# Performance work log

Measured on AMD Instinct MI355X. Metric: run time of the kernel, lower is better.

## Reference

```python
import jax, jax.numpy as jnp
import numpy as np

HEADS = 16
DIM_HEAD = 64
BLOCK = 16
SEQ_LEN = 2048
NUM_BLOCKS = SEQ_LEN // BLOCK  # 128
NUM_RANDOM_BLOCKS = 32
LOCAL_WINDOW = 4
GLOBAL_BLOCKS = [0]


def make_layout():
    # Deterministic stand-in for DeepSpeed VariableSparsityConfig.make_layout
    # (local windows of 4 blocks + random blocks + global block columns/rows,
    #  then tril for unidirectional attention).
    rng = np.random.RandomState(0)
    nb = NUM_BLOCKS
    layout = np.zeros((nb, nb), dtype=bool)
    for w in range(0, nb, LOCAL_WINDOW):
        layout[w:w + LOCAL_WINDOW, w:w + LOCAL_WINDOW] = True
    rnd = rng.randint(0, nb, size=(nb, NUM_RANDOM_BLOCKS))
    layout[np.arange(nb)[:, None], rnd] = True
    for g in GLOBAL_BLOCKS:
        layout[:, g] = True
        layout[g, :] = True
    layout = np.tril(layout)  # unidirectional
    return jnp.asarray(layout)


def setup_inputs() -> dict:
    key = jax.random.key(0)
    k1, k2, k3 = jax.random.split(key, 3)
    dim = 1024
    inner = HEADS * DIM_HEAD  # 1024
    x = jax.random.normal(k1, (2, SEQ_LEN, dim), dtype=jnp.float32)
    w_qkv = jax.random.normal(k2, (dim, 3 * inner), dtype=jnp.float32) * 0.02
    w_out = jax.random.normal(k3, (inner, dim), dtype=jnp.float32) * 0.02
    b_out = jnp.zeros((dim,), dtype=jnp.float32)
    layout = make_layout()  # [128, 128] bool
    return {"x": x, "w_qkv": w_qkv, "w_out": w_out, "b_out": b_out, "layout": layout}


def reference(x, w_qkv, w_out, b_out, layout):
    b, n, _ = x.shape
    scale = DIM_HEAD ** -0.5
    qkv = x @ w_qkv  # [b, n, 3*h*d]
    q, k, v = jnp.split(qkv, 3, axis=-1)
    split_heads = lambda t: t.reshape(b, n, HEADS, DIM_HEAD).transpose(0, 2, 1, 3)
    q, k, v = split_heads(q), split_heads(k), split_heads(v)  # [b, h, n, d]

    scores = jnp.einsum('bhid,bhjd->bhij', q, k) * scale  # [b, h, n, n]
    neg = -jnp.finfo(scores.dtype).max
    # additive causal attn_mask (value = -finfo.max / 2, attn_mask_mode='add')
    causal = jnp.triu(jnp.ones((n, n), dtype=bool), 1)
    scores = scores + jnp.where(causal, neg / 2, jnp.zeros((), scores.dtype))
    # block-sparse layout: entries outside allowed blocks are fully masked
    allowed = jnp.repeat(jnp.repeat(layout, BLOCK, axis=0), BLOCK, axis=1)  # [n, n]
    scores = jnp.where(allowed, scores, neg)
    attn = jax.nn.softmax(scores, axis=-1)
    out = jnp.einsum('bhij,bhjd->bhid', attn, v)  # [b, h, n, d]
    out = out.transpose(0, 2, 1, 3).reshape(b, n, HEADS * DIM_HEAD)
    return out @ w_out + b_out
```

## Files before the change

### kernel.cpp

```cpp
#include <hip/hip_runtime.h>
#include <cstdint>
#include <cstddef>


typedef short bf8 __attribute__((ext_vector_type(8)));
typedef float f32x4 __attribute__((ext_vector_type(4)));
typedef unsigned short u16;
typedef unsigned int u32;

#define MFMA_BF16(a, b, c) __builtin_amdgcn_mfma_f32_16x16x32_bf16((a), (b), (c), 0, 0, 0)

constexpr int SEQ = 2048;
constexpr int NH = 16;
constexpr int DHD = 64;
constexpr int NBLK = 128;
constexpr int DIM = 1024;

__device__ __forceinline__ u16 f2bf(float f) {
  unsigned u = __float_as_uint(f);
  return (u16)((u + 0x7fffu + ((u >> 16) & 1u)) >> 16);
}
__device__ __forceinline__ u32 pack2bf(float a, float b) {
  return (u32)f2bf(a) | ((u32)f2bf(b) << 16);
}
__device__ __forceinline__ void gload_lds16(const u16* g, u16* l) {
  auto gp = (const __attribute__((address_space(1))) u16*)(g);
  auto lp = (__attribute__((address_space(3))) u16*)(l);
  __builtin_amdgcn_global_load_lds(gp, lp, 16, 0, 0);
}

__global__ __launch_bounds__(256) void prep(
    const float* __restrict__ x, u16* __restrict__ xbf,
    const float* __restrict__ wqkv, u16* __restrict__ wqkvT,
    const float* __restrict__ wout, u16* __restrict__ woutT,
    const unsigned char* __restrict__ lay,
    int* __restrict__ cnt, int* __restrict__ cols) {
  __shared__ u16 tile[64][72];
  int bid = blockIdx.x;
  int t = threadIdx.x;

  if (bid < 2048) {
    int idx = (bid * 256 + t) * 8;
    float4 a = *(const float4*)(x + idx);
    float4 b = *(const float4*)(x + idx + 4);
    *(ushort4*)(xbf + idx)     = make_ushort4(f2bf(a.x), f2bf(a.y), f2bf(a.z), f2bf(a.w));
    *(ushort4*)(xbf + idx + 4) = make_ushort4(f2bf(b.x), f2bf(b.y), f2bf(b.z), f2bf(b.w));
    return;
  }
  bid -= 2048;
  if (bid < 768 + 256) {
    const float* in; u16* out; int C, bx, by;
    if (bid < 768) { in = wqkv; out = wqkvT; C = 3072; bx = bid % 48; by = bid / 48; }
    else { int r = bid - 768; in = wout; out = woutT; C = 1024; bx = r % 16; by = r / 16; }
    const int R = 1024;
    int c0 = bx * 64, r0 = by * 64;
    int rr = t >> 4, cc = (t & 15) * 4;
    #pragma unroll
    for (int p = 0; p < 64; p += 16) {
      float4 v = *(const float4*)(in + (size_t)(r0 + rr + p) * C + c0 + cc);
      tile[rr + p][cc + 0] = f2bf(v.x);
      tile[rr + p][cc + 1] = f2bf(v.y);
      tile[rr + p][cc + 2] = f2bf(v.z);
      tile[rr + p][cc + 3] = f2bf(v.w);
    }
    __syncthreads();
    int oc = t >> 3, orr = (t & 7) * 8;
    #pragma unroll
    for (int p = 0; p < 64; p += 32) {
      u16 tmp[8];
      #pragma unroll
      for (int qy = 0; qy < 8; qy++) tmp[qy] = tile[orr + qy][oc + p];
      u16* dst = out + (size_t)(c0 + oc + p) * R + r0 + orr;
      *(ushort4*)(dst)     = make_ushort4(tmp[0], tmp[1], tmp[2], tmp[3]);
      *(ushort4*)(dst + 4) = make_ushort4(tmp[4], tmp[5], tmp[6], tmp[7]);
    }
    return;
  }
  bid -= 1024;
  int wave = t >> 6, lane = t & 63;
  int i = bid * 4 + wave;
  const uint4* l4 = (const uint4*)lay;
  u32 acc = 0;
  #pragma unroll
  for (int it = 0; it < 16; it++) {
    uint4 v = l4[it * 64 + lane];
    acc |= ((v.x | v.y | v.z | v.w) & 0xFFFFFF00u);
  }
  bool as_int32 = (__ballot(acc != 0) == 0ULL);
  const int* li = (const int*)lay;
  int j0 = lane, j1 = lane + 64;
  bool p0 = (j0 <= i) && (as_int32 ? (li[i * 128 + j0] != 0) : (lay[i * 128 + j0] != 0));
  bool p1 = (j1 <= i) && (as_int32 ? (li[i * 128 + j1] != 0) : (lay[i * 128 + j1] != 0));
  unsigned long long m0 = __ballot(p0), m1 = __ballot(p1);
  unsigned long long lt = (1ULL << lane) - 1ULL;
  int base0 = __popcll(m0);
  if (p0) cols[i * 128 + __popcll(m0 & lt)] = j0;
  if (p1) cols[i * 128 + base0 + __popcll(m1 & lt)] = j1;
  if (lane == 0) cnt[i] = base0 + __popcll(m1);
}

__global__ __launch_bounds__(256) void gemm_qkv(
    const u16* __restrict__ A, const u16* __restrict__ Bt,
    u16* __restrict__ oq, u16* __restrict__ okk, u16* __restrict__ ov) {
  __shared__ u16 smem[16896];
  u16* sA = smem;
  u16* sB = smem + 8192;
  const int K = 1024;
  int tid = threadIdx.x, lane = tid & 63, wave = tid >> 6;
  int quad = lane >> 4, l16 = lane & 15;
  int wr = wave >> 1, wc = wave & 1;
  int bm0 = blockIdx.y * 128, bn0 = blockIdx.x * 128;

  f32x4 acc[4][4];
  #pragma unroll
  for (int i = 0; i < 4; i++)
    #pragma unroll
    for (int j = 0; j < 4; j++) acc[i][j] = (f32x4){0.f, 0.f, 0.f, 0.f};

  int srow8 = lane >> 3;
  int schunk = ((lane & 7) ^ srow8) * 8;
  for (int k0 = 0; k0 < K; k0 += 64) {
    #pragma unroll
    for (int r = 0; r < 4; r++) {
      int row = wave * 8 + r * 32 + srow8;
      gload_lds16(A + (size_t)(bm0 + row) * K + k0 + schunk,
                  sA + (wave * 8 + r * 32) * 64);
    }
    #pragma unroll
    for (int r = 0; r < 4; r++) {
      int row = wave * 8 + r * 32 + srow8;
      gload_lds16(Bt + (size_t)(bn0 + row) * K + k0 + schunk,
                  sB + (wave * 8 + r * 32) * 64);
    }
    __syncthreads();
    #pragma unroll
    for (int ks = 0; ks < 2; ks++) {
      bf8 af[4], bfr[4];
      #pragma unroll
      for (int i = 0; i < 4; i++) {
        int phys = ((ks * 4 + quad) ^ (l16 & 7)) * 8;
        af[i] = *(const bf8*)(sA + (wr * 64 + i * 16 + l16) * 64 + phys);
      }
      #pragma unroll
      for (int j = 0; j < 4; j++) {
        int phys = ((ks * 4 + quad) ^ (l16 & 7)) * 8;
        bfr[j] = *(const bf8*)(sB + (wc * 64 + j * 16 + l16) * 64 + phys);
      }
      #pragma unroll
      for (int i = 0; i < 4; i++)
        #pragma unroll
        for (int j = 0; j < 4; j++)
          acc[i][j] = MFMA_BF16(af[i], bfr[j], acc[i][j]);
    }
    __syncthreads();
  }

  int which = bn0 >> 10;
  if (which == 2) {
    #pragma unroll
    for (int j = 0; j < 4; j++) {
      int c = bn0 + wc * 64 + j * 16 + l16;
      int h = (c & 1023) >> 6, dd = c & 63;
      #pragma unroll
      for (int i = 0; i < 4; i++) {
        int r0 = bm0 + wr * 64 + i * 16;
        int b = r0 >> 11, nn0 = r0 & 2047, jb = nn0 >> 4;
        u16* dst = ov + ((size_t)((b * NH + h) * NBLK + jb) * DHD + dd) * 16 + quad * 4;
        *(ushort4*)dst = make_ushort4(f2bf(acc[i][j][0]), f2bf(acc[i][j][1]),
                                      f2bf(acc[i][j][2]), f2bf(acc[i][j][3]));
      }
    }
  } else {
    u16* dstbase = (which == 0) ? oq : okk;
    #pragma unroll
    for (int j = 0; j < 4; j++) {
      int col = wc * 64 + j * 16 + l16;
      #pragma unroll
      for (int i = 0; i < 4; i++) {
        int row = wr * 64 + i * 16 + quad * 4;
        *(uint2*)&smem[col * 132 + row] =
            make_uint2(pack2bf(acc[i][j][0], acc[i][j][1]),
                       pack2bf(acc[i][j][2], acc[i][j][3]));
      }
    }
    __syncthreads();
    int r = tid >> 1, half = tid & 1;
    int rglob = bm0 + r;
    int b = rglob >> 11, nn = rglob & 2047;
    int h = ((bn0 & 1023) >> 6) + half;
    #pragma unroll
    for (int j = 0; j < 4; j++) {
      union { u16 t[16]; uint4 q[2]; } tv;
      #pragma unroll
      for (int dd = 0; dd < 16; dd++)
        tv.t[dd] = smem[(half * 64 + j * 16 + dd) * 132 + r];
      u16* dst = dstbase + ((size_t)(b * NH + h) * SEQ + nn) * DHD + j * 16;
      *(uint4*)(dst) = tv.q[0];
      *(uint4*)(dst + 8) = tv.q[1];
    }
  }
}

__global__ __launch_bounds__(256) void gemm_out(
    const u16* __restrict__ A, const u16* __restrict__ Bt,
    float* __restrict__ of, const float* __restrict__ bias) {
  __shared__ u16 smem[12288];
  u16* sA = smem;
  u16* sB = smem + 8192;
  const int K = 1024, N = 1024;
  int tid = threadIdx.x, lane = tid & 63, wave = tid >> 6;
  int quad = lane >> 4, l16 = lane & 15;
  int wr = wave >> 1, wc = wave & 1;
  int bm0 = blockIdx.y * 128, bn0 = blockIdx.x * 64;

  f32x4 acc[4][2];
  #pragma unroll
  for (int i = 0; i < 4; i++)
    #pragma unroll
    for (int j = 0; j < 2; j++) acc[i][j] = (f32x4){0.f, 0.f, 0.f, 0.f};

  int srow8 = lane >> 3;
  int schunk = ((lane & 7) ^ srow8) * 8;
  for (int k0 = 0; k0 < K; k0 += 64) {
    #pragma unroll
    for (int r = 0; r < 4; r++) {
      int row = wave * 8 + r * 32 + srow8;
      gload_lds16(A + (size_t)(bm0 + row) * K + k0 + schunk,
                  sA + (wave * 8 + r * 32) * 64);
    }
    #pragma unroll
    for (int r = 0; r < 2; r++) {
      int row = wave * 8 + r * 32 + srow8;
      gload_lds16(Bt + (size_t)(bn0 + row) * K + k0 + schunk,
                  sB + (wave * 8 + r * 32) * 64);
    }
    __syncthreads();
    #pragma unroll
    for (int ks = 0; ks < 2; ks++) {
      bf8 af[4], bfr[2];
      #pragma unroll
      for (int i = 0; i < 4; i++) {
        int phys = ((ks * 4 + quad) ^ (l16 & 7)) * 8;
        af[i] = *(const bf8*)(sA + (wr * 64 + i * 16 + l16) * 64 + phys);
      }
      #pragma unroll
      for (int j = 0; j < 2; j++) {
        int phys = ((ks * 4 + quad) ^ (l16 & 7)) * 8;
        bfr[j] = *(const bf8*)(sB + (wc * 32 + j * 16 + l16) * 64 + phys);
      }
      #pragma unroll
      for (int i = 0; i < 4; i++)
        #pragma unroll
        for (int j = 0; j < 2; j++)
          acc[i][j] = MFMA_BF16(af[i], bfr[j], acc[i][j]);
    }
    __syncthreads();
  }

  #pragma unroll
  for (int j = 0; j < 2; j++) {
    int c = bn0 + wc * 32 + j * 16 + l16;
    float bv = bias[c];
    #pragma unroll
    for (int i = 0; i < 4; i++) {
      int rbase = bm0 + wr * 64 + i * 16 + quad * 4;
      #pragma unroll
      for (int ii = 0; ii < 4; ii++)
        of[(size_t)(rbase + ii) * N + c] = acc[i][j][ii] + bv;
    }
  }
}

__global__ __launch_bounds__(256) void attn_sparse(
    const u16* __restrict__ q, const u16* __restrict__ k, const u16* __restrict__ vblk,
    const int* __restrict__ cnt, const int* __restrict__ cols,
    u16* __restrict__ aout) {
  __shared__ u32 pbuf[4][320];
  __shared__ float obuf[2][64 * 20];
  __shared__ float lbuf[2][64];
  int wave = threadIdx.x >> 6, lane = threadIdx.x & 63;
  int quad = lane >> 4, l16 = lane & 15;
  int qslot = wave >> 1, half = wave & 1;
  int blk = blockIdx.x;
  int bh = blk >> 6;
  int qb = (blk & 63) * 2 + qslot;
  const float scale = 0.125f;
  u32* pbw = pbuf[wave];

  const u16* qp = q + ((size_t)bh * SEQ + qb * 16) * DHD + l16 * DHD + quad * 8;
  bf8 qa0 = *(const bf8*)(qp);
  bf8 qa1 = *(const bf8*)(qp + 32);

  float l_i = 0.f;
  f32x4 o[4];
  #pragma unroll
  for (int t = 0; t < 4; t++) o[t] = (f32x4){0.f, 0.f, 0.f, 0.f};

  int count = cnt[qb];
  const int* mc = cols + qb * NBLK;

  bf8 bufA[8], bufB[8];
  int ja0 = 0, ja1 = 0, jb0b = 0, jb1b = 0;
  bool hvA = false, hvB = false;

  auto ldpair = [&](int p, bf8* kv, int& o0, int& o1, bool& ohv) {
    o0 = mc[p];
    ohv = (p + 1 < count);
    o1 = ohv ? mc[p + 1] : o0;
    const u16* kp0 = k + ((size_t)bh * SEQ + o0 * 16) * DHD + l16 * DHD + quad * 8;
    kv[0] = *(const bf8*)(kp0); kv[1] = *(const bf8*)(kp0 + 32);
    const u16* kp1 = k + ((size_t)bh * SEQ + o1 * 16) * DHD + l16 * DHD + quad * 8;
    kv[2] = *(const bf8*)(kp1); kv[3] = *(const bf8*)(kp1 + 32);
    int jq = (quad < 2) ? o0 : o1;
    const u16* vp = vblk + (size_t)(bh * NBLK + jq) * 1024 + l16 * 16 + (quad & 1) * 8;
    kv[4] = *(const bf8*)(vp);
    kv[5] = *(const bf8*)(vp + 256);
    kv[6] = *(const bf8*)(vp + 512);
    kv[7] = *(const bf8*)(vp + 768);
  };

  int myp = half * 2;
  if (myp < count) ldpair(myp, bufA, ja0, ja1, hvA);
  if (myp + 4 < count) ldpair(myp + 4, bufB, jb0b, jb1b, hvB);

  for (int p = myp; p < count; p += 4) {
    f32x4 S0 = (f32x4){0.f, 0.f, 0.f, 0.f};
    S0 = MFMA_BF16(bufA[0], qa0, S0);
    S0 = MFMA_BF16(bufA[1], qa1, S0);
    f32x4 S1 = (f32x4){0.f, 0.f, 0.f, 0.f};
    S1 = MFMA_BF16(bufA[2], qa0, S1);
    S1 = MFMA_BF16(bufA[3], qa1, S1);

    float e0[4], e1[4];
    #pragma unroll
    for (int r = 0; r < 4; r++) {
      int kl = quad * 4 + r;
      float s0 = S0[r] * scale;
      if (ja0 == qb && kl > l16) s0 = -1e38f;
      float s1 = hvA ? S1[r] * scale : -1e38f;
      if (hvA && ja1 == qb && kl > l16) s1 = -1e38f;
      e0[r] = __expf(s0);
      e1[r] = __expf(s1);
      l_i += e0[r] + e1[r];
    }

    *(uint2*)(&pbw[l16 * 20 + quad * 2]) =
        make_uint2(pack2bf(e0[0], e0[1]), pack2bf(e0[2], e0[3]));
    *(uint2*)(&pbw[l16 * 20 + 8 + quad * 2]) =
        make_uint2(pack2bf(e1[0], e1[1]), pack2bf(e1[2], e1[3]));
    union { uint4 w; bf8 v; } pf;
    pf.w = *(const uint4*)(&pbw[l16 * 20 + quad * 4]);

    o[0] = MFMA_BF16(bufA[4], pf.v, o[0]);
    o[1] = MFMA_BF16(bufA[5], pf.v, o[1]);
    o[2] = MFMA_BF16(bufA[6], pf.v, o[2]);
    o[3] = MFMA_BF16(bufA[7], pf.v, o[3]);

    #pragma unroll
    for (int z = 0; z < 8; z++) bufA[z] = bufB[z];
    ja0 = jb0b; ja1 = jb1b; hvA = hvB;
    if (p + 8 < count) ldpair(p + 8, bufB, jb0b, jb1b, hvB);
  }

  if (half == 1) {
    #pragma unroll
    for (int t = 0; t < 4; t++)
      *(f32x4*)(&obuf[qslot][lane * 20 + t * 4]) = o[t];
    lbuf[qslot][lane] = l_i;
  }
  __syncthreads();
  if (half == 0) {
    #pragma unroll
    for (int t = 0; t < 4; t++)
      o[t] += *(const f32x4*)(&obuf[qslot][lane * 20 + t * 4]);
    float l = l_i + lbuf[qslot][lane];
    l += __shfl_xor(l, 16);
    l += __shfl_xor(l, 32);
    float inv = 1.0f / l;
    int b = bh >> 4, h = bh & 15;
    int n = qb * 16 + l16;
    u16* dst = aout + ((size_t)b * SEQ + n) * DIM + h * DHD;
    #pragma unroll
    for (int t = 0; t < 4; t++) {
      ushort4 st = make_ushort4(f2bf(o[t][0] * inv), f2bf(o[t][1] * inv),
                                f2bf(o[t][2] * inv), f2bf(o[t][3] * inv));
      *(ushort4*)(dst + t * 16 + quad * 4) = st;
    }
  }
}

extern "C" void kernel_launch(void* const* d_in, const int* in_sizes, int n_in,
                              void* d_out, int out_size, void* d_ws, size_t ws_size,
                              hipStream_t stream) {
  const float* x      = (const float*)d_in[0];
  const float* w_qkv  = (const float*)d_in[1];
  const float* w_out  = (const float*)d_in[2];
  const float* b_out  = (const float*)d_in[3];
  const unsigned char* layout = (const unsigned char*)d_in[4];
  float* out = (float*)d_out;

  char* ws = (char*)d_ws;
  u16* xbf   = (u16*)(ws);
  u16* wqkvT = (u16*)(ws + (8u  << 20));
  u16* woutT = (u16*)(ws + (14u << 20) + (512u << 10));
  u16* qB    = (u16*)(ws + (17u << 20));
  u16* kB    = (u16*)(ws + (25u << 20));
  u16* vblk  = (u16*)(ws + (33u << 20));
  u16* aout  = (u16*)(ws + (41u << 20));
  int* cnt   = (int*)(ws + (49u << 20));
  int* cols  = (int*)(ws + (49u << 20) + 4096);

  prep<<<3104, 256, 0, stream>>>(x, xbf, w_qkv, wqkvT, w_out, woutT,
                                 layout, cnt, cols);
  gemm_qkv<<<dim3(24, 32, 1), 256, 0, stream>>>(xbf, wqkvT, qB, kB, vblk);
  attn_sparse<<<2048, 256, 0, stream>>>(qB, kB, vblk, cnt, cols, aout);
  gemm_out<<<dim3(16, 32, 1), 256, 0, stream>>>(aout, woutT, out, b_out);
}
```

Before: 180.7 us.

## Swizzle block IDs for XCD locality and split attention keys across four waves

```diff
diff --git a/kernel.cpp b/kernel.cpp
--- a/kernel.cpp
+++ b/kernel.cpp
@@ -109,7 +109,11 @@
   int tid = threadIdx.x, lane = tid & 63, wave = tid >> 6;
   int quad = lane >> 4, l16 = lane & 15;
   int wr = wave >> 1, wc = wave & 1;
-  int bm0 = blockIdx.y * 128, bn0 = blockIdx.x * 128;
+  int d = blockIdx.x;
+  int xcd = d & 7, rest = d >> 3;
+  int bm = xcd + (rest & 3) * 8;
+  int bn = rest >> 2;
+  int bm0 = bm * 128, bn0 = bn * 128;
 
   f32x4 acc[4][4];
   #pragma unroll
@@ -211,7 +215,11 @@
   int tid = threadIdx.x, lane = tid & 63, wave = tid >> 6;
   int quad = lane >> 4, l16 = lane & 15;
   int wr = wave >> 1, wc = wave & 1;
-  int bm0 = blockIdx.y * 128, bn0 = blockIdx.x * 64;
+  int d = blockIdx.x;
+  int xcd = d & 7, slot = d >> 3;
+  int bm = xcd * 4 + (slot & 3);
+  int bn = slot >> 2;
+  int bm0 = bm * 128, bn0 = bn * 64;
 
   f32x4 acc[4][2];
   #pragma unroll
@@ -276,14 +284,14 @@
     const int* __restrict__ cnt, const int* __restrict__ cols,
     u16* __restrict__ aout) {
   __shared__ u32 pbuf[4][320];
-  __shared__ float obuf[2][64 * 20];
-  __shared__ float lbuf[2][64];
+  __shared__ float obuf[3][64 * 20];
+  __shared__ float lbuf[3][64];
   int wave = threadIdx.x >> 6, lane = threadIdx.x & 63;
   int quad = lane >> 4, l16 = lane & 15;
-  int qslot = wave >> 1, half = wave & 1;
   int blk = blockIdx.x;
-  int bh = blk >> 6;
-  int qb = (blk & 63) * 2 + qslot;
+  int xcd = blk & 7, rest = blk >> 3;
+  int bh = xcd * 4 + (rest & 3);
+  int qb = rest >> 2;
   const float scale = 0.125f;
   u32* pbw = pbuf[wave];
 
@@ -319,11 +327,11 @@
     kv[7] = *(const bf8*)(vp + 768);
   };
 
-  int myp = half * 2;
+  int myp = wave * 2;
   if (myp < count) ldpair(myp, bufA, ja0, ja1, hvA);
-  if (myp + 4 < count) ldpair(myp + 4, bufB, jb0b, jb1b, hvB);
-
-  for (int p = myp; p < count; p += 4) {
+  if (myp + 8 < count) ldpair(myp + 8, bufB, jb0b, jb1b, hvB);
+
+  for (int p = myp; p < count; p += 8) {
     f32x4 S0 = (f32x4){0.f, 0.f, 0.f, 0.f};
     S0 = MFMA_BF16(bufA[0], qa0, S0);
     S0 = MFMA_BF16(bufA[1], qa1, S0);
@@ -359,21 +367,25 @@
     #pragma unroll
     for (int z = 0; z < 8; z++) bufA[z] = bufB[z];
     ja0 = jb0b; ja1 = jb1b; hvA = hvB;
-    if (p + 8 < count) ldpair(p + 8, bufB, jb0b, jb1b, hvB);
-  }
-
-  if (half == 1) {
+    if (p + 16 < count) ldpair(p + 16, bufB, jb0b, jb1b, hvB);
+  }
+
+  if (wave > 0) {
     #pragma unroll
     for (int t = 0; t < 4; t++)
-      *(f32x4*)(&obuf[qslot][lane * 20 + t * 4]) = o[t];
-    lbuf[qslot][lane] = l_i;
+      *(f32x4*)(&obuf[wave - 1][lane * 20 + t * 4]) = o[t];
+    lbuf[wave - 1][lane] = l_i;
   }
   __syncthreads();
-  if (half == 0) {
-    #pragma unroll
-    for (int t = 0; t < 4; t++)
-      o[t] += *(const f32x4*)(&obuf[qslot][lane * 20 + t * 4]);
-    float l = l_i + lbuf[qslot][lane];
+  if (wave == 0) {
+    #pragma unroll
+    for (int w = 0; w < 3; w++) {
+      #pragma unroll
+      for (int t = 0; t < 4; t++)
+        o[t] += *(const f32x4*)(&obuf[w][lane * 20 + t * 4]);
+      l_i += lbuf[w][lane];
+    }
+    float l = l_i;
     l += __shfl_xor(l, 16);
     l += __shfl_xor(l, 32);
     float inv = 1.0f / l;
@@ -412,7 +424,7 @@
 
   prep<<<3104, 256, 0, stream>>>(x, xbf, w_qkv, wqkvT, w_out, woutT,
                                  layout, cnt, cols);
-  gemm_qkv<<<dim3(24, 32, 1), 256, 0, stream>>>(xbf, wqkvT, qB, kB, vblk);
-  attn_sparse<<<2048, 256, 0, stream>>>(qB, kB, vblk, cnt, cols, aout);
-  gemm_out<<<dim3(16, 32, 1), 256, 0, stream>>>(aout, woutT, out, b_out);
-}
+  gemm_qkv<<<768, 256, 0, stream>>>(xbf, wqkvT, qB, kB, vblk);
+  attn_sparse<<<4096, 256, 0, stream>>>(qB, kB, vblk, cnt, cols, aout);
+  gemm_out<<<512, 256, 0, stream>>>(aout, woutT, out, b_out);
+}
```

After: 172.1 us. 1.05x faster.
